# Kernel tuning notes

Hardware: AMD Instinct MI355X
Metric: run time of the kernel (lower is better)

The kernel has to match this reference:

```python
import jax, jax.numpy as jnp
import numpy as np
from jax import lax

DIM = 64


def _dwconv(x, w, b):
    # x: [B,C,H,W], w: [C,1,kh,kw] depthwise, 'same' padding
    kh, kw = w.shape[2], w.shape[3]
    y = lax.conv_general_dilated(
        x, w, window_strides=(1, 1),
        padding=[(kh // 2, kh // 2), (kw // 2, kw // 2)],
        dimension_numbers=("NCHW", "OIHW", "NCHW"),
        feature_group_count=x.shape[1])
    return y + b[None, :, None, None]


def _conv1x1(x, w, b):
    y = lax.conv_general_dilated(
        x, w, window_strides=(1, 1), padding="VALID",
        dimension_numbers=("NCHW", "OIHW", "NCHW"))
    return y + b[None, :, None, None]


def _avgpool3(x):
    # PyTorch AvgPool2d(3,1,1) default count_include_pad=True -> sum/9
    s = lax.reduce_window(x, 0.0, lax.add, (1, 1, 3, 3), (1, 1, 1, 1),
                          [(0, 0), (0, 0), (1, 1), (1, 1)])
    return s / 9.0


def _maxpool3(x):
    return lax.reduce_window(x, -jnp.inf, lax.max, (1, 1, 3, 3), (1, 1, 1, 1),
                             [(0, 0), (0, 0), (1, 1), (1, 1)])


def setup_inputs() -> dict:
    key = jax.random.key(0)
    ks = jax.random.split(key, 18)
    C = DIM
    def w(k, shape):
        fan_in = shape[1] * shape[2] * shape[3]
        bound = 1.0 / np.sqrt(fan_in)
        return jax.random.uniform(k, shape, jnp.float32, -bound, bound)
    def b(k, fan_in):
        bound = 1.0 / np.sqrt(fan_in)
        return jax.random.uniform(k, (C,), jnp.float32, -bound, bound)
    return {
        "x": jax.random.normal(ks[0], (16, C, 128, 128), jnp.float32),
        "w55": w(ks[1], (C, 1, 5, 5)), "b55": b(ks[2], 25),
        "w17_0": w(ks[3], (C, 1, 1, 7)), "b17_0": b(ks[4], 7),
        "w17_1": w(ks[5], (C, 1, 7, 1)), "b17_1": b(ks[6], 7),
        "w111_0": w(ks[7], (C, 1, 1, 11)), "b111_0": b(ks[8], 11),
        "w111_1": w(ks[9], (C, 1, 11, 1)), "b111_1": b(ks[10], 11),
        "w211_0": w(ks[11], (C, 1, 1, 21)), "b211_0": b(ks[12], 21),
        "w211_1": w(ks[13], (C, 1, 21, 1)), "b211_1": b(ks[14], 21),
        "w11": w(ks[15], (C, C, 1, 1)), "b11": b(ks[16], C),
    }


def reference(x, w55, b55, w17_0, b17_0, w17_1, b17_1,
              w111_0, b111_0, w111_1, b111_1,
              w211_0, b211_0, w211_1, b211_1, w11, b11):
    def branch(inp):
        c55 = _dwconv(inp, w55, b55)
        c17 = _dwconv(_dwconv(inp, w17_0, b17_0), w17_1, b17_1)
        c111 = _dwconv(_dwconv(inp, w111_0, b111_0), w111_1, b111_1)
        c211 = _dwconv(_dwconv(inp, w211_0, b211_0), w211_1, b211_1)
        return _conv1x1(c55 + c17 + c111 + c211, w11, b11)

    mixer = branch(x)
    mixer_1 = branch(_avgpool3(x))
    mixer_2 = branch(_maxpool3(x))
    return (mixer + mixer_1 + mixer_2) * x
```

## Files before the change

kernel.cpp:

```cpp
#include <hip/hip_runtime.h>
#include <cstdint>

#define HH 128
#define WW 128
#define CC 64
#define BB 16
#define PLANE (HH*WW)

#define XS_OFF    0
#define XS_STR    60
#define XST_OFF   5040
#define XST_STR   68
#define H7_OFF    7488
#define H7_STR    76
#define UNION_OFF 9920
#define XRAW_STR  60
#define H11_OFF   UNION_OFF
#define H11_STR   76
#define H21_OFF   (UNION_OFF + 2432)
#define H21_STR   92
#define SMEM_FLOATS 15296

__global__ __launch_bounds__(256) void k_dwsum(
    const float* __restrict__ x, float* __restrict__ T,
    const float* __restrict__ w55, const float* __restrict__ b55,
    const float* __restrict__ w17_0, const float* __restrict__ b17_0,
    const float* __restrict__ w17_1, const float* __restrict__ b17_1,
    const float* __restrict__ w111_0, const float* __restrict__ b111_0,
    const float* __restrict__ w111_1, const float* __restrict__ b111_1,
    const float* __restrict__ w211_0, const float* __restrict__ b211_0,
    const float* __restrict__ w211_1, const float* __restrict__ b211_1) {
  __shared__ float sm[SMEM_FLOATS];

  const int bid = blockIdx.x;
  const int pl = bid >> 3;
  const int t = bid & 7;
  const int tR0 = (t >> 2) * 64;
  const int tC0 = (t & 3) * 32;
  const int ch = pl & (CC - 1);
  const float* xp = x + (size_t)pl * PLANE;
  float* Tp = T + (size_t)pl * PLANE;
  const int tid = threadIdx.x;

  {
    float* xraw = sm + UNION_OFF;
    const int base_r = tR0 - 11, base_c = tC0 - 12;
    for (int i = tid; i < 86 * 14; i += 256) {
      int rr = i / 14;
      int jj = i - rr * 14;
      int gr = base_r + rr;
      int gc = base_c + jj * 4;
      float4 v = make_float4(0.f, 0.f, 0.f, 0.f);
      if ((unsigned)gr < 128u && (unsigned)gc < 128u)
        v = *(const float4*)(xp + gr * WW + gc);
      *(float4*)(xraw + rr * XRAW_STR + jj * 4) = v;
    }
  }
  __syncthreads();

  {
    const float* xraw = sm + UNION_OFF;
    for (int i = tid; i < 84 * 13; i += 256) {
      int rr = i / 13;
      int jj = i - rr * 13;
      const float* rp = xraw + rr * XRAW_STR + jj * 4;
      float4 a0 = *(const float4*)(rp);
      float4 a1 = *(const float4*)(rp + 4);
      float4 b0 = *(const float4*)(rp + XRAW_STR);
      float4 b1 = *(const float4*)(rp + XRAW_STR + 4);
      float4 c0 = *(const float4*)(rp + 2 * XRAW_STR);
      float4 c1 = *(const float4*)(rp + 2 * XRAW_STR + 4);
      float w0[8] = {a0.x, a0.y, a0.z, a0.w, a1.x, a1.y, a1.z, a1.w};
      float w1[8] = {b0.x, b0.y, b0.z, b0.w, b1.x, b1.y, b1.z, b1.w};
      float w2[8] = {c0.x, c0.y, c0.z, c0.w, c1.x, c1.y, c1.z, c1.w};
      int gr = tR0 + rr - 10;
      bool rv0 = (unsigned)(gr - 1) < 128u;
      bool rv1 = (unsigned)(gr) < 128u;
      bool rv2 = (unsigned)(gr + 1) < 128u;
      int gc0 = tC0 + jj * 4 - 12;
      float M0[8], M1[8], M2[8];
      #pragma unroll
      for (int p = 1; p <= 6; ++p) {
        bool cv = (unsigned)(gc0 + p) < 128u;
        M0[p] = (rv0 && cv) ? w0[p] : -3.402823466e38f;
        M1[p] = (rv1 && cv) ? w1[p] : -3.402823466e38f;
        M2[p] = (rv2 && cv) ? w2[p] : -3.402823466e38f;
      }
      float uq[4];
      #pragma unroll
      for (int q = 0; q < 4; ++q) {
        float s = w0[q + 1] + w0[q + 2] + w0[q + 3] + w1[q + 1] + w1[q + 2] +
                  w1[q + 3] + w2[q + 1] + w2[q + 2] + w2[q + 3];
        float m = fmaxf(
            fmaxf(fmaxf(M0[q + 1], M0[q + 2]), fmaxf(M0[q + 3], M1[q + 1])),
            fmaxf(fmaxf(M1[q + 2], M1[q + 3]),
                  fmaxf(fmaxf(M2[q + 1], M2[q + 2]), M2[q + 3])));
        float val = w1[q + 2] + s * (1.f / 9.f) + m;
        bool vo = rv1 && ((unsigned)(gc0 + q + 2) < 128u);
        uq[q] = vo ? val : 0.f;
      }
      *(float4*)(sm + XS_OFF + rr * XS_STR + jj * 4) =
          make_float4(uq[0], uq[1], uq[2], uq[3]);
      int rt = rr - 8;
      if ((unsigned)rt < 68u) {
        #pragma unroll
        for (int q = 0; q < 4; ++q) {
          int ct = jj * 4 + q - 8;
          if ((unsigned)ct < 36u) sm[XST_OFF + ct * XST_STR + rt] = uq[q];
        }
      }
    }
  }

  float k7[7], k11[11], k21[21];
  #pragma unroll
  for (int i = 0; i < 7; ++i) k7[i] = w17_0[ch * 7 + i];
  #pragma unroll
  for (int i = 0; i < 11; ++i) k11[i] = w111_0[ch * 11 + i];
  #pragma unroll
  for (int i = 0; i < 21; ++i) k21[i] = w211_0[ch * 21 + i];
  float bb7 = 3.f * b17_0[ch];
  float bb11 = 3.f * b111_0[ch];
  float bb21 = 3.f * b211_0[ch];

  __syncthreads();

  for (int it = tid; it < 84 * 4; it += 256) {
    int rr = it >> 2;
    int cg = it & 3;
    float w[28];
    const float* xr = sm + XS_OFF + rr * XS_STR + cg * 8;
    #pragma unroll
    for (int j = 0; j < 7; ++j) {
      float4 v = *(const float4*)(xr + 4 * j);
      w[4 * j] = v.x; w[4 * j + 1] = v.y; w[4 * j + 2] = v.z; w[4 * j + 3] = v.w;
    }
    int gr = tR0 + rr - 10;
    bool rv = (unsigned)gr < 128u;
    bool v11r = (rr >= 5) && (rr <= 78);
    bool v7r = (rr >= 7) && (rr <= 76);
    #pragma unroll
    for (int j = 0; j < 8; ++j) {
      float a21 = bb21, a11 = bb11, a7 = bb7;
      #pragma unroll
      for (int d = 0; d < 21; ++d) a21 += k21[d] * w[j + d];
      #pragma unroll
      for (int d = 0; d < 11; ++d) a11 += k11[d] * w[j + 5 + d];
      #pragma unroll
      for (int d = 0; d < 7; ++d) a7 += k7[d] * w[j + 7 + d];
      int c = cg * 8 + j;
      sm[H21_OFF + c * H21_STR + rr] = rv ? a21 : 0.f;
      if (v11r) sm[H11_OFF + c * H11_STR + rr - 5] = rv ? a11 : 0.f;
      if (v7r) sm[H7_OFF + c * H7_STR + rr - 7] = rv ? a7 : 0.f;
    }
  }

  float v7a[7], v11a[11], v21a[21], w5a[25];
  #pragma unroll
  for (int i = 0; i < 7; ++i) v7a[i] = w17_1[ch * 7 + i];
  #pragma unroll
  for (int i = 0; i < 11; ++i) v11a[i] = w111_1[ch * 11 + i];
  #pragma unroll
  for (int i = 0; i < 21; ++i) v21a[i] = w211_1[ch * 21 + i];
  #pragma unroll
  for (int i = 0; i < 25; ++i) w5a[i] = w55[ch * 25 + i];
  float bsum = 3.f * (b55[ch] + b17_1[ch] + b111_1[ch] + b211_1[ch]);

  __syncthreads();

  {
    int c = tid & 31;
    int r0 = (tid >> 5) * 8;
    float acc[8];
    #pragma unroll
    for (int j = 0; j < 8; ++j) acc[j] = bsum;

    float A[28];
    {
      const float* hp = sm + H21_OFF + c * H21_STR + r0;
      #pragma unroll
      for (int j = 0; j < 7; ++j) {
        float4 v = *(const float4*)(hp + 4 * j);
        A[4 * j] = v.x; A[4 * j + 1] = v.y; A[4 * j + 2] = v.z; A[4 * j + 3] = v.w;
      }
      #pragma unroll
      for (int d = 0; d < 21; ++d)
        #pragma unroll
        for (int j = 0; j < 8; ++j) acc[j] += v21a[d] * A[d + j];
    }
    {
      const float* hp = sm + H11_OFF + c * H11_STR + r0;
      #pragma unroll
      for (int j = 0; j < 5; ++j) {
        float4 v = *(const float4*)(hp + 4 * j);
        A[4 * j] = v.x; A[4 * j + 1] = v.y; A[4 * j + 2] = v.z; A[4 * j + 3] = v.w;
      }
      #pragma unroll
      for (int d = 0; d < 11; ++d)
        #pragma unroll
        for (int j = 0; j < 8; ++j) acc[j] += v11a[d] * A[d + j];
    }
    {
      const float* hp = sm + H7_OFF + c * H7_STR + r0;
      #pragma unroll
      for (int j = 0; j < 4; ++j) {
        float4 v = *(const float4*)(hp + 4 * j);
        A[4 * j] = v.x; A[4 * j + 1] = v.y; A[4 * j + 2] = v.z; A[4 * j + 3] = v.w;
      }
      #pragma unroll
      for (int d = 0; d < 7; ++d)
        #pragma unroll
        for (int j = 0; j < 8; ++j) acc[j] += v7a[d] * A[d + j];
    }
    #pragma unroll
    for (int dc = 0; dc < 5; ++dc) {
      const float* hp = sm + XST_OFF + (c + dc) * XST_STR + r0;
      float X[12];
      #pragma unroll
      for (int j = 0; j < 3; ++j) {
        float4 v = *(const float4*)(hp + 4 * j);
        X[4 * j] = v.x; X[4 * j + 1] = v.y; X[4 * j + 2] = v.z; X[4 * j + 3] = v.w;
      }
      #pragma unroll
      for (int dr = 0; dr < 5; ++dr)
        #pragma unroll
        for (int j = 0; j < 8; ++j) acc[j] += w5a[dr * 5 + dc] * X[j + dr];
    }
    #pragma unroll
    for (int j = 0; j < 8; ++j)
      Tp[(size_t)(tR0 + r0 + j) * WW + tC0 + c] = acc[j];
  }
}

__global__ __launch_bounds__(256) void k_mix(const float* __restrict__ T,
                                             const float* __restrict__ x,
                                             const float* __restrict__ w11,
                                             const float* __restrict__ b11,
                                             float* __restrict__ out) {
  __shared__ float Wt[64 * 68];
  int bid = blockIdx.x;
  int b = bid >> 6;
  int px0 = (bid & 63) * 256;
  int tid = threadIdx.x;

  for (int i = tid; i < 4096; i += 256) {
    int co = i >> 6, ci = i & 63;
    Wt[ci * 68 + co] = w11[i];
  }
  __syncthreads();

  int pxg = tid & 31;
  int cog = tid >> 5;
  const float* Tb = T + (size_t)b * (CC * PLANE) + px0 + pxg * 8;
  const float* wrow = Wt + cog * 8;

  float acc[8][8];
  #pragma unroll
  for (int a = 0; a < 8; ++a)
    #pragma unroll
    for (int p = 0; p < 8; ++p) acc[a][p] = 0.f;

  #pragma unroll 4
  for (int k = 0; k < 64; ++k) {
    float4 t0 = *(const float4*)(Tb + (size_t)k * PLANE);
    float4 t1 = *(const float4*)(Tb + (size_t)k * PLANE + 4);
    float4 q0 = *(const float4*)(wrow + k * 68);
    float4 q1 = *(const float4*)(wrow + k * 68 + 4);
    float tv[8] = {t0.x, t0.y, t0.z, t0.w, t1.x, t1.y, t1.z, t1.w};
    float wf[8] = {q0.x, q0.y, q0.z, q0.w, q1.x, q1.y, q1.z, q1.w};
    #pragma unroll
    for (int a = 0; a < 8; ++a)
      #pragma unroll
      for (int p = 0; p < 8; ++p) acc[a][p] += wf[a] * tv[p];
  }

  const float* xb = x + (size_t)b * (CC * PLANE) + px0 + pxg * 8;
  float* ob = out + (size_t)b * (CC * PLANE) + px0 + pxg * 8;
  #pragma unroll
  for (int a = 0; a < 8; ++a) {
    int co = cog * 8 + a;
    float bb = 3.f * b11[co];
    const float* xr = xb + (size_t)co * PLANE;
    float* orow = ob + (size_t)co * PLANE;
    float4 x0 = *(const float4*)(xr);
    float4 x1 = *(const float4*)(xr + 4);
    float4 o0, o1;
    o0.x = (acc[a][0] + bb) * x0.x; o0.y = (acc[a][1] + bb) * x0.y;
    o0.z = (acc[a][2] + bb) * x0.z; o0.w = (acc[a][3] + bb) * x0.w;
    o1.x = (acc[a][4] + bb) * x1.x; o1.y = (acc[a][5] + bb) * x1.y;
    o1.z = (acc[a][6] + bb) * x1.z; o1.w = (acc[a][7] + bb) * x1.w;
    *(float4*)(orow) = o0;
    *(float4*)(orow + 4) = o1;
  }
}

extern "C" void kernel_launch(void* const* d_in, const int* in_sizes, int n_in,
                              void* d_out, int out_size, void* d_ws,
                              size_t ws_size, hipStream_t stream) {
  const float* x = (const float*)d_in[0];
  const float* w55 = (const float*)d_in[1];
  const float* b55 = (const float*)d_in[2];
  const float* w17_0 = (const float*)d_in[3];
  const float* b17_0 = (const float*)d_in[4];
  const float* w17_1 = (const float*)d_in[5];
  const float* b17_1 = (const float*)d_in[6];
  const float* w111_0 = (const float*)d_in[7];
  const float* b111_0 = (const float*)d_in[8];
  const float* w111_1 = (const float*)d_in[9];
  const float* b111_1 = (const float*)d_in[10];
  const float* w211_0 = (const float*)d_in[11];
  const float* b211_0 = (const float*)d_in[12];
  const float* w211_1 = (const float*)d_in[13];
  const float* b211_1 = (const float*)d_in[14];
  const float* w11 = (const float*)d_in[15];
  const float* b11 = (const float*)d_in[16];
  float* outp = (float*)d_out;

  float* T = (float*)d_ws;

  k_dwsum<<<BB * CC * 8, 256, 0, stream>>>(
      x, T, w55, b55, w17_0, b17_0, w17_1, b17_1, w111_0, b111_0, w111_1,
      b111_1, w211_0, b211_0, w211_1, b211_1);
  k_mix<<<BB * 64, 256, 0, stream>>>(T, x, w11, b11, outp);
}
```

Before: 331.9 us.

## Store 5x5 transposed tile as bf16, shrink LDS, rework mix kernel tiling with prefetch

The depthwise kernel now keeps the transposed input tile for the 5x5 conv in bf16 and unpacks it with shifts, and it tightens the LDS strides so each block uses less shared memory. It also asks for 3 blocks per CU, and the row/column index mapping for the stencil loops changes. The 1x1 mix kernel switches to 128-pixel blocks with 4 pixels per thread, doubles the grid, and software-prefetches T in chunks of 4 channels. The bf16 storage lowers precision of the 5x5 branch input, and the index remap may change LDS bank-conflict behaviour.

```diff
diff --git a/kernel.cpp b/kernel.cpp
--- a/kernel.cpp
+++ b/kernel.cpp
@@ -1,4 +1,5 @@
 #include <hip/hip_runtime.h>
+#include <hip/hip_bf16.h>
 #include <cstdint>
 
 #define HH 128
@@ -8,20 +9,26 @@
 #define PLANE (HH*WW)
 
 #define XS_OFF    0
-#define XS_STR    60
-#define XST_OFF   5040
-#define XST_STR   68
-#define H7_OFF    7488
-#define H7_STR    76
-#define UNION_OFF 9920
-#define XRAW_STR  60
+#define XS_STR    56
+#define XSTH_OFF  4704
+#define H7_OFF    6000
+#define H7_STR    72
+#define UNION_OFF 8304
+#define XRAW_STR  56
 #define H11_OFF   UNION_OFF
 #define H11_STR   76
 #define H21_OFF   (UNION_OFF + 2432)
-#define H21_STR   92
-#define SMEM_FLOATS 15296
-
-__global__ __launch_bounds__(256) void k_dwsum(
+#define H21_STR   84
+#define SMEM_FLOATS 13424
+
+__device__ __forceinline__ float lo16(unsigned int u) {
+  return __uint_as_float(u << 16);
+}
+__device__ __forceinline__ float hi16(unsigned int u) {
+  return __uint_as_float(u & 0xffff0000u);
+}
+
+__global__ __launch_bounds__(256, 3) void k_dwsum(
     const float* __restrict__ x, float* __restrict__ T,
     const float* __restrict__ w55, const float* __restrict__ b55,
     const float* __restrict__ w17_0, const float* __restrict__ b17_0,
@@ -60,9 +67,10 @@
 
   {
     const float* xraw = sm + UNION_OFF;
+    __hip_bfloat16* xsTh = (__hip_bfloat16*)(sm + XSTH_OFF);
     for (int i = tid; i < 84 * 13; i += 256) {
-      int rr = i / 13;
-      int jj = i - rr * 13;
+      int rr = i % 84;
+      int jj = i / 84;
       const float* rp = xraw + rr * XRAW_STR + jj * 4;
       float4 a0 = *(const float4*)(rp);
       float4 a1 = *(const float4*)(rp + 4);
@@ -106,7 +114,8 @@
         #pragma unroll
         for (int q = 0; q < 4; ++q) {
           int ct = jj * 4 + q - 8;
-          if ((unsigned)ct < 36u) sm[XST_OFF + ct * XST_STR + rt] = uq[q];
+          if ((unsigned)ct < 36u)
+            xsTh[ct * 72 + rt] = __float2bfloat16(uq[q]);
         }
       }
     }
@@ -126,8 +135,8 @@
   __syncthreads();
 
   for (int it = tid; it < 84 * 4; it += 256) {
-    int rr = it >> 2;
-    int cg = it & 3;
+    int rr = it % 84;
+    int cg = it / 84;
     float w[28];
     const float* xr = sm + XS_OFF + rr * XS_STR + cg * 8;
     #pragma unroll
@@ -212,19 +221,25 @@
         #pragma unroll
         for (int j = 0; j < 8; ++j) acc[j] += v7a[d] * A[d + j];
     }
-    #pragma unroll
-    for (int dc = 0; dc < 5; ++dc) {
-      const float* hp = sm + XST_OFF + (c + dc) * XST_STR + r0;
-      float X[12];
-      #pragma unroll
-      for (int j = 0; j < 3; ++j) {
-        float4 v = *(const float4*)(hp + 4 * j);
-        X[4 * j] = v.x; X[4 * j + 1] = v.y; X[4 * j + 2] = v.z; X[4 * j + 3] = v.w;
-      }
-      #pragma unroll
-      for (int dr = 0; dr < 5; ++dr)
-        #pragma unroll
-        for (int j = 0; j < 8; ++j) acc[j] += w5a[dr * 5 + dc] * X[j + dr];
+    {
+      const unsigned int* xp32 = (const unsigned int*)(sm + XSTH_OFF);
+      #pragma unroll
+      for (int dc = 0; dc < 5; ++dc) {
+        const unsigned int* hp = xp32 + (((c + dc) * 72 + r0) >> 1);
+        uint4 u = *(const uint4*)hp;
+        uint2 u2 = *(const uint2*)(hp + 4);
+        float X[12];
+        X[0] = lo16(u.x);  X[1] = hi16(u.x);
+        X[2] = lo16(u.y);  X[3] = hi16(u.y);
+        X[4] = lo16(u.z);  X[5] = hi16(u.z);
+        X[6] = lo16(u.w);  X[7] = hi16(u.w);
+        X[8] = lo16(u2.x); X[9] = hi16(u2.x);
+        X[10] = lo16(u2.y); X[11] = hi16(u2.y);
+        #pragma unroll
+        for (int dr = 0; dr < 5; ++dr)
+          #pragma unroll
+          for (int j = 0; j < 8; ++j) acc[j] += w5a[dr * 5 + dc] * X[j + dr];
+      }
     }
     #pragma unroll
     for (int j = 0; j < 8; ++j)
@@ -232,15 +247,15 @@
   }
 }
 
-__global__ __launch_bounds__(256) void k_mix(const float* __restrict__ T,
-                                             const float* __restrict__ x,
-                                             const float* __restrict__ w11,
-                                             const float* __restrict__ b11,
-                                             float* __restrict__ out) {
+__global__ __launch_bounds__(256, 4) void k_mix(const float* __restrict__ T,
+                                                const float* __restrict__ x,
+                                                const float* __restrict__ w11,
+                                                const float* __restrict__ b11,
+                                                float* __restrict__ out) {
   __shared__ float Wt[64 * 68];
   int bid = blockIdx.x;
-  int b = bid >> 6;
-  int px0 = (bid & 63) * 256;
+  int b = bid >> 7;
+  int px0 = (bid & 127) * 128;
   int tid = threadIdx.x;
 
   for (int i = tid; i < 4096; i += 256) {
@@ -251,46 +266,57 @@
 
   int pxg = tid & 31;
   int cog = tid >> 5;
-  const float* Tb = T + (size_t)b * (CC * PLANE) + px0 + pxg * 8;
-  const float* wrow = Wt + cog * 8;
-
-  float acc[8][8];
+  const float* Tb = T + (size_t)b * (CC * PLANE) + px0 + pxg * 4;
+  const float* wp = Wt + cog * 8;
+
+  float acc[8][4];
   #pragma unroll
   for (int a = 0; a < 8; ++a)
     #pragma unroll
-    for (int p = 0; p < 8; ++p) acc[a][p] = 0.f;
-
-  #pragma unroll 4
-  for (int k = 0; k < 64; ++k) {
-    float4 t0 = *(const float4*)(Tb + (size_t)k * PLANE);
-    float4 t1 = *(const float4*)(Tb + (size_t)k * PLANE + 4);
-    float4 q0 = *(const float4*)(wrow + k * 68);
-    float4 q1 = *(const float4*)(wrow + k * 68 + 4);
-    float tv[8] = {t0.x, t0.y, t0.z, t0.w, t1.x, t1.y, t1.z, t1.w};
-    float wf[8] = {q0.x, q0.y, q0.z, q0.w, q1.x, q1.y, q1.z, q1.w};
-    #pragma unroll
-    for (int a = 0; a < 8; ++a)
-      #pragma unroll
-      for (int p = 0; p < 8; ++p) acc[a][p] += wf[a] * tv[p];
-  }
-
-  const float* xb = x + (size_t)b * (CC * PLANE) + px0 + pxg * 8;
-  float* ob = out + (size_t)b * (CC * PLANE) + px0 + pxg * 8;
+    for (int p = 0; p < 4; ++p) acc[a][p] = 0.f;
+
+  float4 tb[2][4];
+  #pragma unroll
+  for (int kk = 0; kk < 4; ++kk)
+    tb[0][kk] = *(const float4*)(Tb + (size_t)kk * PLANE);
+
+  #pragma unroll
+  for (int kc = 0; kc < 16; ++kc) {
+    const int cur = kc & 1;
+    if (kc < 15) {
+      #pragma unroll
+      for (int kk = 0; kk < 4; ++kk)
+        tb[cur ^ 1][kk] =
+            *(const float4*)(Tb + (size_t)((kc + 1) * 4 + kk) * PLANE);
+    }
+    #pragma unroll
+    for (int kk = 0; kk < 4; ++kk) {
+      int k = kc * 4 + kk;
+      float4 q0 = *(const float4*)(wp + k * 68);
+      float4 q1 = *(const float4*)(wp + k * 68 + 4);
+      float wf[8] = {q0.x, q0.y, q0.z, q0.w, q1.x, q1.y, q1.z, q1.w};
+      float4 tv = tb[cur][kk];
+      float tvv[4] = {tv.x, tv.y, tv.z, tv.w};
+      #pragma unroll
+      for (int a = 0; a < 8; ++a)
+        #pragma unroll
+        for (int p = 0; p < 4; ++p) acc[a][p] += wf[a] * tvv[p];
+    }
+  }
+
+  const float* xb = x + (size_t)b * (CC * PLANE) + px0 + pxg * 4;
+  float* ob = out + (size_t)b * (CC * PLANE) + px0 + pxg * 4;
   #pragma unroll
   for (int a = 0; a < 8; ++a) {
     int co = cog * 8 + a;
     float bb = 3.f * b11[co];
-    const float* xr = xb + (size_t)co * PLANE;
-    float* orow = ob + (size_t)co * PLANE;
-    float4 x0 = *(const float4*)(xr);
-    float4 x1 = *(const float4*)(xr + 4);
-    float4 o0, o1;
-    o0.x = (acc[a][0] + bb) * x0.x; o0.y = (acc[a][1] + bb) * x0.y;
-    o0.z = (acc[a][2] + bb) * x0.z; o0.w = (acc[a][3] + bb) * x0.w;
-    o1.x = (acc[a][4] + bb) * x1.x; o1.y = (acc[a][5] + bb) * x1.y;
-    o1.z = (acc[a][6] + bb) * x1.z; o1.w = (acc[a][7] + bb) * x1.w;
-    *(float4*)(orow) = o0;
-    *(float4*)(orow + 4) = o1;
+    float4 xv = *(const float4*)(xb + (size_t)co * PLANE);
+    float4 o;
+    o.x = (acc[a][0] + bb) * xv.x;
+    o.y = (acc[a][1] + bb) * xv.y;
+    o.z = (acc[a][2] + bb) * xv.z;
+    o.w = (acc[a][3] + bb) * xv.w;
+    *(float4*)(ob + (size_t)co * PLANE) = o;
   }
 }
 
@@ -321,5 +347,5 @@
   k_dwsum<<<BB * CC * 8, 256, 0, stream>>>(
       x, T, w55, b55, w17_0, b17_0, w17_1, b17_1, w111_0, b111_0, w111_1,
       b111_1, w211_0, b211_0, w211_1, b211_1);
-  k_mix<<<BB * 64, 256, 0, stream>>>(T, x, w11, b11, outp);
-}
+  k_mix<<<BB * 128, 256, 0, stream>>>(T, x, w11, b11, outp);
+}
```

After: 306.6 us. 1.08x faster.
